# Optimization experiments

Measured on AMD Instinct MI355X. Metric: run time of the kernel, lower is better.

## Reference

```python
import jax, jax.numpy as jnp
import numpy as np

B, S, H, NH = 2, 2048, 1024, 16
DK = H // NH

def setup_inputs() -> dict:
    key = jax.random.key(0)
    ks = jax.random.split(key, 12)
    scale = 0.02
    return {
        "Q": jax.random.normal(ks[0], (B, S, H), jnp.float32),
        "K": jax.random.normal(ks[1], (B, S, H), jnp.float32),
        "V": jax.random.normal(ks[2], (B, S, H), jnp.float32),
        "attn_mask": jax.random.randint(ks[3], (B, S, S), 0, 2).astype(bool),
        "Wq": jax.random.normal(ks[4], (H, H), jnp.float32) * scale,
        "bq": jnp.zeros((H,), jnp.float32),
        "Wk": jax.random.normal(ks[5], (H, H), jnp.float32) * scale,
        "bk": jnp.zeros((H,), jnp.float32),
        "Wv": jax.random.normal(ks[6], (H, H), jnp.float32) * scale,
        "bv": jnp.zeros((H,), jnp.float32),
        "Wo": jax.random.normal(ks[7], (H, H), jnp.float32) * scale,
        "bo": jnp.zeros((H,), jnp.float32),
    }

def reference(Q, K, V, attn_mask, Wq, bq, Wk, bk, Wv, bv, Wo, bo):
    b = Q.shape[0]
    # linear projections (torch nn.Linear: x @ W.T + b), split heads -> [b, nh, s, dk]
    def proj(x, W, bias):
        return (x @ W.T + bias).reshape(b, -1, NH, DK).transpose(0, 2, 1, 3)
    q = proj(Q, Wq, bq)
    k = proj(K, Wk, bk)
    v = proj(V, Wv, bv)
    scores = jnp.einsum("bhqd,bhkd->bhqk", q, k) / jnp.sqrt(jnp.float32(DK))
    scores = jnp.where(attn_mask[:, None, :, :], jnp.float32(-1e9), scores)
    attn = jax.nn.softmax(scores, axis=-1)  # dropout prob = 0.0 (identity)
    ctx = jnp.einsum("bhqk,bhkd->bhqd", attn, v)
    ctx = ctx.transpose(0, 2, 1, 3).reshape(b, -1, NH * DK)
    return ctx @ Wo.T + bo
```

## Files before the change

### kernel.cpp

```cpp
#include <hip/hip_runtime.h>
#include <hip/hip_bf16.h>

typedef short s16x8 __attribute__((ext_vector_type(8)));
typedef float f32x4 __attribute__((ext_vector_type(4)));
typedef unsigned short u16;
typedef unsigned int u32;
typedef unsigned long long u64;

#define DEVI __device__ __forceinline__

#if __has_builtin(__builtin_amdgcn_exp2f)
#define EXP2F(x) __builtin_amdgcn_exp2f(x)
#else
#define EXP2F(x) exp2f(x)
#endif

#define QSCALE 0.1803368801111204f

DEVI float bf2f(u16 u){ union { u32 i; float f; } v; v.i = ((u32)u) << 16; return v.f; }
DEVI u16 f2bf(float f){ union { float f; u32 i; } v; v.f = f; u32 u = v.i;
                        return (u16)((u + 0x7fffu + ((u >> 16) & 1u)) >> 16); }

DEVI u32 pkbf2(float a, float b){
  union { __hip_bfloat162 h; u32 u; } v;
  v.h = __float22bfloat162_rn(make_float2(a, b));
  return v.u;
}
DEVI u64 pk4(float a, float b, float c, float d){
  return (u64)pkbf2(a, b) | ((u64)pkbf2(c, d) << 32);
}

DEVI f32x4 mfma_bf16(s16x8 a, s16x8 b, f32x4 c){
  return __builtin_amdgcn_mfma_f32_16x16x32_bf16(a, b, c, 0, 0, 0);
}

#define GLDS(gp, lp) __builtin_amdgcn_global_load_lds( \
    (const __attribute__((address_space(1))) void*)(gp), \
    (__attribute__((address_space(3))) void*)(lp), 16, 0, 0)

DEVI float4 cvt8f32(const float* p){
  float4 x = *(const float4*)p;
  float4 y = *(const float4*)(p + 4);
  union { u32 t[4]; float4 f4; } u;
  u.t[0] = pkbf2(x.x, x.y); u.t[1] = pkbf2(x.z, x.w);
  u.t[2] = pkbf2(y.x, y.y); u.t[3] = pkbf2(y.z, y.w);
  return u.f4;
}

DEVI bool detect_f32(const u16* probe){
  __shared__ int dsum[4];
  const int tid = threadIdx.x;
  int bad = 0;
#pragma unroll
  for (int i = 0; i < 16; ++i){
    u16 u = probe[tid * 16 + i];
    int e = (u >> 7) & 0xFF;
    bad += (e != 0 && (e < 100 || e > 150)) ? 1 : 0;
  }
#pragma unroll
  for (int o = 1; o < 64; o <<= 1) bad += __shfl_xor(bad, o);
  if ((tid & 63) == 0) dsum[tid >> 6] = bad;
  __syncthreads();
  bool r = (dsum[0] + dsum[1] + dsum[2] + dsum[3]) > 64;
  __syncthreads();
  return r;
}

struct PrepArgs { const void* src[7]; void* dst[7]; u32 coff[8]; };

__global__ __launch_bounds__(256) void prep_mask(PrepArgs a, const u16* probe,
                                                 const int* __restrict__ mask,
                                                 u64* __restrict__ bits,
                                                 int do_mask, int do_conv){
  if (blockIdx.x < 1024){
    if (!do_mask) return;
    const int lane = threadIdx.x & 63, wid = threadIdx.x >> 6;
    const int row = blockIdx.x * 4 + wid;
    const int* mrow = mask + (size_t)row * 2048;
    for (int c = 0; c < 32; ++c){
      int v = mrow[c * 64 + lane];
      u64 w = __ballot(v == 0);
      if (lane == 0) bits[(size_t)row * 32 + c] = w;
    }
  } else {
    if (!do_conv) return;
    const bool f32 = detect_f32(probe);
    if (!f32) return;
    const u32 total = a.coff[7];
    for (u32 c = (blockIdx.x - 1024) * 256 + threadIdx.x; c < total; c += 2048 * 256){
      int s = 0;
#pragma unroll
      for (int i = 1; i < 7; ++i) s += (c >= a.coff[i]) ? 1 : 0;
      u32 lc = c - a.coff[s];
      ((float4*)a.dst[s])[lc] = cvt8f32((const float*)a.src[s] + (size_t)lc * 8);
    }
  }
}

struct ProjP {
  const void* X[3];   const u16* Xc[3];
  const void* W[3];   const u16* Wc[3];
  const void* bias[3];
  u16* out[3];
  const u16* probe;
  int conv_ok;
};

__global__ __launch_bounds__(256) void proj_gemm(ProjP p){
  __shared__ u16 As[128 * 64];
  __shared__ u16 Bs[128 * 64];
  const int z = blockIdx.z;
  const bool in32 = detect_f32(p.probe);
  const bool f32st = in32 && !p.conv_ok;
  const u16* Ab = (in32 && p.conv_ok) ? p.Xc[z] : (const u16*)p.X[z];
  const u16* Wb = (in32 && p.conv_ok) ? p.Wc[z] : (const u16*)p.W[z];
  const float* Af = (const float*)p.X[z];
  const float* Wf = (const float*)p.W[z];
  const int tid = threadIdx.x;
  const int lane = tid & 63, wid = tid >> 6;
  const int quad = lane >> 4, l15 = lane & 15;
  const int m0 = blockIdx.y * 128, n0 = blockIdx.x * 128;
  const int wm = (wid >> 1) * 64, wn = (wid & 1) * 64;
  const int K = 1024;

  f32x4 acc[4][4];
  const f32x4 z4 = {0.f, 0.f, 0.f, 0.f};
  for (int i = 0; i < 4; ++i) for (int j = 0; j < 4; ++j) acc[i][j] = z4;

  for (int ko = 0; ko < 16; ++ko){
    const int kk = ko * 64;
    if (f32st){
#pragma unroll
      for (int i = 0; i < 4; ++i){
        int g = tid * 4 + i;
        int row = g >> 3, c = g & 7;
        *(float4*)(As + row * 64 + ((c ^ (row & 7)) * 8)) =
            cvt8f32(Af + (size_t)(m0 + row) * K + kk + c * 8);
        *(float4*)(Bs + row * 64 + ((c ^ (row & 7)) * 8)) =
            cvt8f32(Wf + (size_t)(n0 + row) * K + kk + c * 8);
      }
    } else {
#pragma unroll
      for (int i = 0; i < 4; ++i){
        int ci = (wid * 4 + i) * 64 + lane;
        int row = ci >> 3, gcc = (ci & 7) ^ (row & 7);
        GLDS(Ab + (size_t)(m0 + row) * K + kk + gcc * 8, As + (size_t)(wid * 4 + i) * 512);
        GLDS(Wb + (size_t)(n0 + row) * K + kk + gcc * 8, Bs + (size_t)(wid * 4 + i) * 512);
      }
    }
    __syncthreads();
#pragma unroll
    for (int ks = 0; ks < 2; ++ks){
      s16x8 af[4], bfr[4];
#pragma unroll
      for (int mt = 0; mt < 4; ++mt){
        int row = wm + mt * 16 + l15;
        af[mt] = *(const s16x8*)(As + row * 64 + (((ks * 4 + quad) ^ (row & 7)) * 8));
      }
#pragma unroll
      for (int nt = 0; nt < 4; ++nt){
        int row = wn + nt * 16 + l15;
        bfr[nt] = *(const s16x8*)(Bs + row * 64 + (((ks * 4 + quad) ^ (row & 7)) * 8));
      }
#pragma unroll
      for (int mt = 0; mt < 4; ++mt)
#pragma unroll
        for (int nt = 0; nt < 4; ++nt)
          acc[mt][nt] = mfma_bf16(af[mt], bfr[nt], acc[mt][nt]);
    }
    __syncthreads();
  }

  u16* outp = p.out[z];
#pragma unroll
  for (int nt = 0; nt < 4; ++nt){
    int col = n0 + wn + nt * 16 + l15;
    float bv = in32 ? ((const float*)p.bias[z])[col] : bf2f(((const u16*)p.bias[z])[col]);
#pragma unroll
    for (int mt = 0; mt < 4; ++mt){
      if (z == 2){
        int srow = m0 + wm + mt * 16 + quad * 4;
        int b = srow >> 11, s = srow & 2047, hh = col >> 6, d = col & 63;
        size_t idx = (((size_t)(b * 16 + hh)) * 64 + d) * 2048 + s;
        *(u64*)(outp + idx) = pk4(acc[mt][nt][0] + bv, acc[mt][nt][1] + bv,
                                  acc[mt][nt][2] + bv, acc[mt][nt][3] + bv);
      } else {
#pragma unroll
        for (int r = 0; r < 4; ++r){
          int row = m0 + wm + mt * 16 + quad * 4 + r;
          float v = acc[mt][nt][r] + bv;
          if (z == 0) v *= QSCALE;
          int b = row >> 11, s = row & 2047, hh = col >> 6, d = col & 63;
          outp[(((size_t)(b * 16 + hh)) * 2048 + s) * 64 + d] = f2bf(v);
        }
      }
    }
  }
}

__global__ __launch_bounds__(256) void gemm_out(const u16* __restrict__ A,
                                                const void* __restrict__ Wv,
                                                const u16* __restrict__ Wbf,
                                                const void* __restrict__ biasv,
                                                void* __restrict__ outv,
                                                const u16* __restrict__ probe,
                                                int conv_ok){
  __shared__ u16 As[64 * 64];
  __shared__ u16 Bs[64 * 64];
  const bool in32 = detect_f32(probe);
  const bool f32st = in32 && !conv_ok;
  const u16* Wb = (in32 && conv_ok) ? Wbf : (const u16*)Wv;
  const float* Wf = (const float*)Wv;
  const int tid = threadIdx.x;
  const int lane = tid & 63, wid = tid >> 6;
  const int quad = lane >> 4, l15 = lane & 15;
  const int m0 = blockIdx.y * 64, n0 = blockIdx.x * 64;
  const int wm = (wid >> 1) * 32, wn = (wid & 1) * 32;
  const int K = 1024;

  f32x4 acc[2][2];
  const f32x4 z4 = {0.f, 0.f, 0.f, 0.f};
  for (int i = 0; i < 2; ++i) for (int j = 0; j < 2; ++j) acc[i][j] = z4;

  for (int ko = 0; ko < 16; ++ko){
    const int kk = ko * 64;
#pragma unroll
    for (int i = 0; i < 2; ++i){
      int ci = (wid * 2 + i) * 64 + lane;
      int row = ci >> 3, gcc = (ci & 7) ^ (row & 7);
      GLDS(A + (size_t)(m0 + row) * K + kk + gcc * 8, As + (size_t)(wid * 2 + i) * 512);
    }
    if (f32st){
#pragma unroll
      for (int i = 0; i < 2; ++i){
        int g = tid * 2 + i;
        int row = g >> 3, c = g & 7;
        *(float4*)(Bs + row * 64 + ((c ^ (row & 7)) * 8)) =
            cvt8f32(Wf + (size_t)(n0 + row) * K + kk + c * 8);
      }
    } else {
#pragma unroll
      for (int i = 0; i < 2; ++i){
        int ci = (wid * 2 + i) * 64 + lane;
        int row = ci >> 3, gcc = (ci & 7) ^ (row & 7);
        GLDS(Wb + (size_t)(n0 + row) * K + kk + gcc * 8, Bs + (size_t)(wid * 2 + i) * 512);
      }
    }
    __syncthreads();
#pragma unroll
    for (int ks = 0; ks < 2; ++ks){
      s16x8 af[2], bfr[2];
#pragma unroll
      for (int mt = 0; mt < 2; ++mt){
        int row = wm + mt * 16 + l15;
        af[mt] = *(const s16x8*)(As + row * 64 + (((ks * 4 + quad) ^ (row & 7)) * 8));
      }
#pragma unroll
      for (int nt = 0; nt < 2; ++nt){
        int row = wn + nt * 16 + l15;
        bfr[nt] = *(const s16x8*)(Bs + row * 64 + (((ks * 4 + quad) ^ (row & 7)) * 8));
      }
#pragma unroll
      for (int mt = 0; mt < 2; ++mt)
#pragma unroll
        for (int nt = 0; nt < 2; ++nt)
          acc[mt][nt] = mfma_bf16(af[mt], bfr[nt], acc[mt][nt]);
    }
    __syncthreads();
  }

#pragma unroll
  for (int nt = 0; nt < 2; ++nt){
    int col = n0 + wn + nt * 16 + l15;
    float bv = in32 ? ((const float*)biasv)[col] : bf2f(((const u16*)biasv)[col]);
#pragma unroll
    for (int mt = 0; mt < 2; ++mt)
#pragma unroll
      for (int r = 0; r < 4; ++r){
        int row = m0 + wm + mt * 16 + quad * 4 + r;
        float v = acc[mt][nt][r] + bv;
        size_t idx = (size_t)row * 1024 + col;
        if (in32) ((float*)outv)[idx] = v;
        else      ((u16*)outv)[idx]   = f2bf(v);
      }
  }
}

__global__ __launch_bounds__(256, 2) void attn2(const u16* __restrict__ qws,
                                                const u16* __restrict__ kws,
                                                const u16* __restrict__ vtws,
                                                const u64* __restrict__ mbits,
                                                const int* __restrict__ rawmask,
                                                int use_raw,
                                                u16* __restrict__ ctxws){
  __shared__ u16 Ks[2][64 * 64];
  __shared__ u16 Vt[2][64 * 64];
  __shared__ u16 Ps[4][32 * 64];
  const int tid = threadIdx.x;
  const int lane = tid & 63, wid = tid >> 6;
  const int quad = lane >> 4, l15 = lane & 15;
  const int h = blockIdx.x, qt = blockIdx.y, b = blockIdx.z;
  const int q0 = qt * 128;
  const size_t bh = (size_t)(b * 16 + h) * (2048 * 64);
  int qrow[2];
  qrow[0] = q0 + wid * 32 + l15;
  qrow[1] = qrow[0] + 16;

  s16x8 qf[2][2];
#pragma unroll
  for (int rg = 0; rg < 2; ++rg)
#pragma unroll
    for (int ks = 0; ks < 2; ++ks)
      qf[rg][ks] = *(const s16x8*)(qws + bh + (size_t)qrow[rg] * 64 + ks * 32 + quad * 8);

  const f32x4 z4 = {0.f, 0.f, 0.f, 0.f};
  f32x4 ctx[2][4];
#pragma unroll
  for (int rg = 0; rg < 2; ++rg)
    for (int dt = 0; dt < 4; ++dt) ctx[rg][dt] = z4;
  float lr[2] = {0.f, 0.f};

  u16* pp = &Ps[wid][0];
  u32 pw[2][4];
#pragma unroll
  for (int rg = 0; rg < 2; ++rg)
#pragma unroll
    for (int ntk = 0; ntk < 4; ++ntk)
      pw[rg][ntk] = (rg * 16 + l15) * 64 +
                    (((u32)(ntk * 2 + (quad >> 1)) ^ (u32)(l15 & 7)) * 8) + (quad & 1) * 4;

  const u64* mrow0 = mbits + ((size_t)(b * 2048 + qrow[0])) * 32;
  const u64* mrow1 = mbits + ((size_t)(b * 2048 + qrow[1])) * 32;

  const int sci = wid * 2;
  int srow0, sgc0, srow1, sgc1;
  {
    int ci0 = sci * 64 + lane;
    srow0 = ci0 >> 3; sgc0 = (ci0 & 7) ^ (srow0 & 7);
    int ci1 = (sci + 1) * 64 + lane;
    srow1 = ci1 >> 3; sgc1 = (ci1 & 7) ^ (srow1 & 7);
  }
  const u16* kp0 = kws + bh + (size_t)srow0 * 64 + sgc0 * 8;
  const u16* kp1 = kws + bh + (size_t)srow1 * 64 + sgc1 * 8;
  const u16* vp0 = vtws + bh + (size_t)srow0 * 2048 + sgc0 * 8;
  const u16* vp1 = vtws + bh + (size_t)srow1 * 2048 + sgc1 * 8;

  GLDS(kp0, &Ks[0][0] + (size_t)sci * 512);
  GLDS(vp0, &Vt[0][0] + (size_t)sci * 512);
  GLDS(kp1, &Ks[0][0] + (size_t)(sci + 1) * 512);
  GLDS(vp1, &Vt[0][0] + (size_t)(sci + 1) * 512);
  kp0 += 4096; kp1 += 4096; vp0 += 64; vp1 += 64;

  for (int kt = 0; kt < 32; kt += 2){
#pragma unroll
    for (int hb = 0; hb < 2; ++hb){
      const int t = kt + hb;
      const u16* kb = &Ks[hb][0];
      const u16* vb = &Vt[hb][0];
      __syncthreads();

      u64 mw0 = 0, mw1 = 0;
      if (!use_raw){ mw0 = mrow0[t]; mw1 = mrow1[t]; }

      if (t < 31){
        u16* kd = &Ks[hb ^ 1][0];
        u16* vd = &Vt[hb ^ 1][0];
        GLDS(kp0, kd + (size_t)sci * 512);
        GLDS(vp0, vd + (size_t)sci * 512);
        GLDS(kp1, kd + (size_t)(sci + 1) * 512);
        GLDS(vp1, vd + (size_t)(sci + 1) * 512);
        kp0 += 4096; kp1 += 4096; vp0 += 64; vp1 += 64;
      }

      f32x4 s[2][4];
#pragma unroll
      for (int rg = 0; rg < 2; ++rg)
#pragma unroll
        for (int ntk = 0; ntk < 4; ++ntk) s[rg][ntk] = z4;
#pragma unroll
      for (int ks = 0; ks < 2; ++ks)
#pragma unroll
        for (int ntk = 0; ntk < 4; ++ntk){
          int row = ntk * 16 + l15;
          s16x8 kf = *(const s16x8*)(kb + row * 64 + (((ks * 4 + quad) ^ (row & 7)) * 8));
          s[0][ntk] = mfma_bf16(kf, qf[0][ks], s[0][ntk]);
          s[1][ntk] = mfma_bf16(kf, qf[1][ks], s[1][ntk]);
        }

      if (!use_raw){
#pragma unroll
        for (int rg = 0; rg < 2; ++rg){
          u64 w = (rg ? mw1 : mw0) >> (quad * 4);
          u32 wlo = (u32)w, whi = (u32)(w >> 32);
          float ls = 0.f;
#pragma unroll
          for (int ntk = 0; ntk < 4; ++ntk){
            u32 half32 = (ntk < 2) ? wlo : whi;
#pragma unroll
            for (int r = 0; r < 4; ++r){
              u32 keep = half32 & (1u << ((ntk & 1) * 16 + r));
              float sv = keep ? s[rg][ntk][r] : -1.0e9f;
              float pv = EXP2F(sv);
              s[rg][ntk][r] = pv;
              ls += pv;
            }
          }
          lr[rg] += ls;
        }
      } else {
        const int k0 = t * 64;
#pragma unroll
        for (int rg = 0; rg < 2; ++rg){
          float ls = 0.f;
#pragma unroll
          for (int ntk = 0; ntk < 4; ++ntk)
#pragma unroll
            for (int r = 0; r < 4; ++r){
              int key = k0 + ntk * 16 + quad * 4 + r;
              int mv = rawmask[((size_t)(b * 2048 + qrow[rg])) * 2048 + key];
              float pv = EXP2F(mv ? -1.0e9f : s[rg][ntk][r]);
              s[rg][ntk][r] = pv;
              ls += pv;
            }
          lr[rg] += ls;
        }
      }

#pragma unroll
      for (int rg = 0; rg < 2; ++rg)
#pragma unroll
        for (int ntk = 0; ntk < 4; ++ntk){
          uint2 tt;
          tt.x = pkbf2(s[rg][ntk][0], s[rg][ntk][1]);
          tt.y = pkbf2(s[rg][ntk][2], s[rg][ntk][3]);
          *(uint2*)(pp + pw[rg][ntk]) = tt;
        }
      s16x8 pf[2][2];
#pragma unroll
      for (int rg = 0; rg < 2; ++rg)
#pragma unroll
        for (int ks = 0; ks < 2; ++ks)
          pf[rg][ks] = *(const s16x8*)(pp + (rg * 16 + l15) * 64 +
                                       (((ks * 4 + quad) ^ (l15 & 7)) * 8));

#pragma unroll
      for (int ks = 0; ks < 2; ++ks)
#pragma unroll
        for (int dt = 0; dt < 4; ++dt){
          int row = dt * 16 + l15;
          s16x8 vf = *(const s16x8*)(vb + row * 64 + (((ks * 4 + quad) ^ (row & 7)) * 8));
          ctx[0][dt] = mfma_bf16(vf, pf[0][ks], ctx[0][dt]);
          ctx[1][dt] = mfma_bf16(vf, pf[1][ks], ctx[1][dt]);
        }
    }
  }

#pragma unroll
  for (int rg = 0; rg < 2; ++rg){
    lr[rg] += __shfl_xor(lr[rg], 16);
    lr[rg] += __shfl_xor(lr[rg], 32);
    float inv = 1.0f / fmaxf(lr[rg], 1e-30f);
#pragma unroll
    for (int dt = 0; dt < 4; ++dt){
      int d0 = dt * 16 + quad * 4;
      u64 w = pk4(ctx[rg][dt][0] * inv, ctx[rg][dt][1] * inv,
                  ctx[rg][dt][2] * inv, ctx[rg][dt][3] * inv);
      *(u64*)(ctxws + ((size_t)(b * 2048 + qrow[rg])) * 1024 + h * 64 + d0) = w;
    }
  }
}

extern "C" void kernel_launch(void* const* d_in, const int* in_sizes, int n_in,
                              void* d_out, int out_size, void* d_ws, size_t ws_size,
                              hipStream_t stream){
  const void* Q    = d_in[0];
  const void* Kin  = d_in[1];
  const void* Vin  = d_in[2];
  const int* mask  = (const int*)d_in[3];
  const void* Wq = d_in[4];  const void* bq = d_in[5];
  const void* Wk = d_in[6];  const void* bk = d_in[7];
  const void* Wv = d_in[8];  const void* bv = d_in[9];
  const void* Wo = d_in[10]; const void* bo = d_in[11];

  char* ws = (char*)d_ws;
  const size_t MB = 1u << 20;
  const bool small_ws = ws_size < 33 * MB;
  const bool big_ws   = ws_size >= 66 * MB;
  u64* mbits = (u64*)ws;
  const size_t base = small_ws ? 0 : MB;
  u16* qws  = (u16*)(ws + base);
  u16* kws  = (u16*)(ws + base + 8 * MB);
  u16* vtws = (u16*)(ws + base + 16 * MB);
  u16* cws  = (u16*)(ws + base + 24 * MB);
  u16* Qc  = (u16*)(ws + 33 * MB);
  u16* Kc  = (u16*)(ws + 41 * MB);
  u16* Vc  = (u16*)(ws + 49 * MB);
  u16* Wqc = (u16*)(ws + 57 * MB);
  u16* Wkc = (u16*)(ws + 59 * MB);
  u16* Wvc = (u16*)(ws + 61 * MB);
  u16* Woc = (u16*)(ws + 63 * MB);
  const u16* probe = (const u16*)Q;

  PrepArgs pa;
  pa.src[0] = Q;  pa.src[1] = Kin; pa.src[2] = Vin;
  pa.src[3] = Wq; pa.src[4] = Wk;  pa.src[5] = Wv; pa.src[6] = Wo;
  pa.dst[0] = Qc;  pa.dst[1] = Kc;  pa.dst[2] = Vc;
  pa.dst[3] = Wqc; pa.dst[4] = Wkc; pa.dst[5] = Wvc; pa.dst[6] = Woc;
  const u32 cq = 4194304 / 8, cw = 1048576 / 8;
  pa.coff[0] = 0;
  pa.coff[1] = cq;          pa.coff[2] = 2 * cq;      pa.coff[3] = 3 * cq;
  pa.coff[4] = 3 * cq + cw; pa.coff[5] = 3 * cq + 2 * cw;
  pa.coff[6] = 3 * cq + 3 * cw; pa.coff[7] = 3 * cq + 4 * cw;
  prep_mask<<<dim3(3072), 256, 0, stream>>>(pa, probe, mask, mbits,
                                            small_ws ? 0 : 1, big_ws ? 1 : 0);

  ProjP pp;
  pp.X[0] = Q;  pp.X[1] = Kin; pp.X[2] = Vin;
  pp.Xc[0] = Qc; pp.Xc[1] = Kc; pp.Xc[2] = Vc;
  pp.W[0] = Wq; pp.W[1] = Wk; pp.W[2] = Wv;
  pp.Wc[0] = Wqc; pp.Wc[1] = Wkc; pp.Wc[2] = Wvc;
  pp.bias[0] = bq; pp.bias[1] = bk; pp.bias[2] = bv;
  pp.out[0] = qws; pp.out[1] = kws; pp.out[2] = vtws;
  pp.probe = probe;
  pp.conv_ok = big_ws ? 1 : 0;
  proj_gemm<<<dim3(8, 32, 3), 256, 0, stream>>>(pp);

  attn2<<<dim3(16, 16, 2), 256, 0, stream>>>(qws, kws, vtws, mbits, mask,
                                             small_ws ? 1 : 0, cws);

  gemm_out<<<dim3(16, 64), 256, 0, stream>>>(cws, Wo, Woc, bo, d_out, probe,
                                             big_ws ? 1 : 0);
}
```

Measured before the change: 279.7 us.

## Load K/V fragments straight to registers, drop LDS staging and barriers

Result: slower. 346.2 us (+23.8%).

```diff
diff --git a/kernel.cpp b/kernel.cpp
--- a/kernel.cpp
+++ b/kernel.cpp
@@ -286,6 +286,111 @@
   }
 }
 
+#define ATT_TILE(T, KC, KN)                                                   \
+  do {                                                                        \
+    const int t_ = (T);                                                       \
+    u64 mw0 = 0, mw1 = 0;                                                     \
+    if (!use_raw){ mw0 = mrow0[t_]; mw1 = mrow1[t_]; }                        \
+       \
+    s16x8 vf[8];                                                              \
+    {                                                                         \
+      const u16* vtb = vbp + (size_t)t_ * 64;                                 \
+      _Pragma("unroll")                                                       \
+      for (int ks = 0; ks < 2; ++ks)                                          \
+        _Pragma("unroll")                                                     \
+        for (int dt = 0; dt < 4; ++dt)                                        \
+          vf[ks * 4 + dt] = *(const s16x8*)(vtb + vo[dt] + ks * 32);          \
+    }                                                                         \
+    f32x4 sv[2][4];                                                           \
+    _Pragma("unroll")                                                         \
+    for (int rg = 0; rg < 2; ++rg)                                            \
+      _Pragma("unroll")                                                       \
+      for (int n = 0; n < 4; ++n) sv[rg][n] = z4;                             \
+    __builtin_amdgcn_s_setprio(1);                                            \
+    _Pragma("unroll")                                                         \
+    for (int ks = 0; ks < 2; ++ks)                                            \
+      _Pragma("unroll")                                                       \
+      for (int n = 0; n < 4; ++n){                                            \
+        sv[0][n] = mfma_bf16(KC[ks * 4 + n], qf[0][ks], sv[0][n]);            \
+        sv[1][n] = mfma_bf16(KC[ks * 4 + n], qf[1][ks], sv[1][n]);            \
+      }                                                                       \
+    __builtin_amdgcn_s_setprio(0);                                            \
+        \
+    {                                                                         \
+      const u16* knb = kbp + (size_t)(t_ + 1) * 4096;                         \
+      _Pragma("unroll")                                                       \
+      for (int ks = 0; ks < 2; ++ks)                                          \
+        _Pragma("unroll")                                                     \
+        for (int n = 0; n < 4; ++n)                                           \
+          KN[ks * 4 + n] = *(const s16x8*)(knb + ko[n] + ks * 32);            \
+    }                                                                         \
+                \
+    if (!use_raw){                                                            \
+      _Pragma("unroll")                                                       \
+      for (int rg = 0; rg < 2; ++rg){                                         \
+        u64 w = (rg ? mw1 : mw0) >> (quad * 4);                               \
+        u32 wlo = (u32)w, whi = (u32)(w >> 32);                               \
+        float ls = 0.f;                                                       \
+        _Pragma("unroll")                                                     \
+        for (int n = 0; n < 4; ++n){                                          \
+          u32 half32 = (n < 2) ? wlo : whi;                                   \
+          _Pragma("unroll")                                                   \
+          for (int r = 0; r < 4; ++r){                                        \
+            u32 keep = half32 & (1u << ((n & 1) * 16 + r));                   \
+            float svv = keep ? sv[rg][n][r] : -1.0e9f;                        \
+            float pv = EXP2F(svv);                                            \
+            sv[rg][n][r] = pv;                                                \
+            ls += pv;                                                         \
+          }                                                                   \
+        }                                                                     \
+        lr[rg] += ls;                                                         \
+      }                                                                       \
+    } else {                                                                  \
+      const int k0 = t_ * 64;                                                 \
+      _Pragma("unroll")                                                       \
+      for (int rg = 0; rg < 2; ++rg){                                         \
+        float ls = 0.f;                                                       \
+        _Pragma("unroll")                                                     \
+        for (int n = 0; n < 4; ++n)                                           \
+          _Pragma("unroll")                                                   \
+          for (int r = 0; r < 4; ++r){                                        \
+            int key = k0 + n * 16 + quad * 4 + r;                             \
+            int mv = rawmask[((size_t)(b * 2048 + qrow[rg])) * 2048 + key];   \
+            float pv = EXP2F(mv ? -1.0e9f : sv[rg][n][r]);                    \
+            sv[rg][n][r] = pv;                                                \
+            ls += pv;                                                         \
+          }                                                                   \
+        lr[rg] += ls;                                                         \
+      }                                                                       \
+    }                                                                         \
+                        \
+    _Pragma("unroll")                                                         \
+    for (int rg = 0; rg < 2; ++rg)                                            \
+      _Pragma("unroll")                                                       \
+      for (int n = 0; n < 4; ++n){                                            \
+        uint2 tt;                                                             \
+        tt.x = pkbf2(sv[rg][n][0], sv[rg][n][1]);                             \
+        tt.y = pkbf2(sv[rg][n][2], sv[rg][n][3]);                             \
+        *(uint2*)(pp + pw[rg][n]) = tt;                                       \
+      }                                                                       \
+    s16x8 pf[2][2];                                                           \
+    _Pragma("unroll")                                                         \
+    for (int rg = 0; rg < 2; ++rg)                                            \
+      _Pragma("unroll")                                                       \
+      for (int ks = 0; ks < 2; ++ks)                                          \
+        pf[rg][ks] = *(const s16x8*)(pp + (rg * 16 + l15) * 64 +              \
+                                     (((ks * 4 + quad) ^ (l15 & 7)) * 8));    \
+    __builtin_amdgcn_s_setprio(1);                                            \
+    _Pragma("unroll")                                                         \
+    for (int ks = 0; ks < 2; ++ks)                                            \
+      _Pragma("unroll")                                                       \
+      for (int dt = 0; dt < 4; ++dt){                                         \
+        ctx[0][dt] = mfma_bf16(vf[ks * 4 + dt], pf[0][ks], ctx[0][dt]);       \
+        ctx[1][dt] = mfma_bf16(vf[ks * 4 + dt], pf[1][ks], ctx[1][dt]);       \
+      }                                                                       \
+    __builtin_amdgcn_s_setprio(0);                                            \
+  } while (0)
+
 __global__ __launch_bounds__(256, 2) void attn2(const u16* __restrict__ qws,
                                                 const u16* __restrict__ kws,
                                                 const u16* __restrict__ vtws,
@@ -293,13 +398,13 @@
                                                 const int* __restrict__ rawmask,
                                                 int use_raw,
                                                 u16* __restrict__ ctxws){
-  __shared__ u16 Ks[2][64 * 64];
-  __shared__ u16 Vt[2][64 * 64];
   __shared__ u16 Ps[4][32 * 64];
   const int tid = threadIdx.x;
   const int lane = tid & 63, wid = tid >> 6;
   const int quad = lane >> 4, l15 = lane & 15;
-  const int h = blockIdx.x, qt = blockIdx.y, b = blockIdx.z;
+  const int bid = blockIdx.x;
+  const int p = bid & 31, qt = bid >> 5;
+  const int h = p & 15, b = p >> 4;
   const int q0 = qt * 128;
   const size_t bh = (size_t)(b * 16 + h) * (2048 * 64);
   int qrow[2];
@@ -332,127 +437,25 @@
   const u64* mrow0 = mbits + ((size_t)(b * 2048 + qrow[0])) * 32;
   const u64* mrow1 = mbits + ((size_t)(b * 2048 + qrow[1])) * 32;
 
-  const int sci = wid * 2;
-  int srow0, sgc0, srow1, sgc1;
-  {
-    int ci0 = sci * 64 + lane;
-    srow0 = ci0 >> 3; sgc0 = (ci0 & 7) ^ (srow0 & 7);
-    int ci1 = (sci + 1) * 64 + lane;
-    srow1 = ci1 >> 3; sgc1 = (ci1 & 7) ^ (srow1 & 7);
-  }
-  const u16* kp0 = kws + bh + (size_t)srow0 * 64 + sgc0 * 8;
-  const u16* kp1 = kws + bh + (size_t)srow1 * 64 + sgc1 * 8;
-  const u16* vp0 = vtws + bh + (size_t)srow0 * 2048 + sgc0 * 8;
-  const u16* vp1 = vtws + bh + (size_t)srow1 * 2048 + sgc1 * 8;
-
-  GLDS(kp0, &Ks[0][0] + (size_t)sci * 512);
-  GLDS(vp0, &Vt[0][0] + (size_t)sci * 512);
-  GLDS(kp1, &Ks[0][0] + (size_t)(sci + 1) * 512);
-  GLDS(vp1, &Vt[0][0] + (size_t)(sci + 1) * 512);
-  kp0 += 4096; kp1 += 4096; vp0 += 64; vp1 += 64;
+  const u16* kbp = kws + bh;
+  const u16* vbp = vtws + bh;
+  u32 ko[4], vo[4];
+#pragma unroll
+  for (int i = 0; i < 4; ++i){
+    ko[i] = (u32)(i * 16 + l15) * 64 + quad * 8;
+    vo[i] = (u32)(i * 16 + l15) * 2048 + quad * 8;
+  }
+
+  s16x8 kfa[8], kfb[8];
+#pragma unroll
+  for (int ks = 0; ks < 2; ++ks)
+#pragma unroll
+    for (int n = 0; n < 4; ++n)
+      kfa[ks * 4 + n] = *(const s16x8*)(kbp + ko[n] + ks * 32);
 
   for (int kt = 0; kt < 32; kt += 2){
-#pragma unroll
-    for (int hb = 0; hb < 2; ++hb){
-      const int t = kt + hb;
-      const u16* kb = &Ks[hb][0];
-      const u16* vb = &Vt[hb][0];
-      __syncthreads();
-
-      u64 mw0 = 0, mw1 = 0;
-      if (!use_raw){ mw0 = mrow0[t]; mw1 = mrow1[t]; }
-
-      if (t < 31){
-        u16* kd = &Ks[hb ^ 1][0];
-        u16* vd = &Vt[hb ^ 1][0];
-        GLDS(kp0, kd + (size_t)sci * 512);
-        GLDS(vp0, vd + (size_t)sci * 512);
-        GLDS(kp1, kd + (size_t)(sci + 1) * 512);
-        GLDS(vp1, vd + (size_t)(sci + 1) * 512);
-        kp0 += 4096; kp1 += 4096; vp0 += 64; vp1 += 64;
-      }
-
-      f32x4 s[2][4];
-#pragma unroll
-      for (int rg = 0; rg < 2; ++rg)
-#pragma unroll
-        for (int ntk = 0; ntk < 4; ++ntk) s[rg][ntk] = z4;
-#pragma unroll
-      for (int ks = 0; ks < 2; ++ks)
-#pragma unroll
-        for (int ntk = 0; ntk < 4; ++ntk){
-          int row = ntk * 16 + l15;
-          s16x8 kf = *(const s16x8*)(kb + row * 64 + (((ks * 4 + quad) ^ (row & 7)) * 8));
-          s[0][ntk] = mfma_bf16(kf, qf[0][ks], s[0][ntk]);
-          s[1][ntk] = mfma_bf16(kf, qf[1][ks], s[1][ntk]);
-        }
-
-      if (!use_raw){
-#pragma unroll
-        for (int rg = 0; rg < 2; ++rg){
-          u64 w = (rg ? mw1 : mw0) >> (quad * 4);
-          u32 wlo = (u32)w, whi = (u32)(w >> 32);
-          float ls = 0.f;
-#pragma unroll
-          for (int ntk = 0; ntk < 4; ++ntk){
-            u32 half32 = (ntk < 2) ? wlo : whi;
-#pragma unroll
-            for (int r = 0; r < 4; ++r){
-              u32 keep = half32 & (1u << ((ntk & 1) * 16 + r));
-              float sv = keep ? s[rg][ntk][r] : -1.0e9f;
-              float pv = EXP2F(sv);
-              s[rg][ntk][r] = pv;
-              ls += pv;
-            }
-          }
-          lr[rg] += ls;
-        }
-      } else {
-        const int k0 = t * 64;
-#pragma unroll
-        for (int rg = 0; rg < 2; ++rg){
-          float ls = 0.f;
-#pragma unroll
-          for (int ntk = 0; ntk < 4; ++ntk)
-#pragma unroll
-            for (int r = 0; r < 4; ++r){
-              int key = k0 + ntk * 16 + quad * 4 + r;
-              int mv = rawmask[((size_t)(b * 2048 + qrow[rg])) * 2048 + key];
-              float pv = EXP2F(mv ? -1.0e9f : s[rg][ntk][r]);
-              s[rg][ntk][r] = pv;
-              ls += pv;
-            }
-          lr[rg] += ls;
-        }
-      }
-
-#pragma unroll
-      for (int rg = 0; rg < 2; ++rg)
-#pragma unroll
-        for (int ntk = 0; ntk < 4; ++ntk){
-          uint2 tt;
-          tt.x = pkbf2(s[rg][ntk][0], s[rg][ntk][1]);
-          tt.y = pkbf2(s[rg][ntk][2], s[rg][ntk][3]);
-          *(uint2*)(pp + pw[rg][ntk]) = tt;
-        }
-      s16x8 pf[2][2];
-#pragma unroll
-      for (int rg = 0; rg < 2; ++rg)
-#pragma unroll
-        for (int ks = 0; ks < 2; ++ks)
-          pf[rg][ks] = *(const s16x8*)(pp + (rg * 16 + l15) * 64 +
-                                       (((ks * 4 + quad) ^ (l15 & 7)) * 8));
-
-#pragma unroll
-      for (int ks = 0; ks < 2; ++ks)
-#pragma unroll
-        for (int dt = 0; dt < 4; ++dt){
-          int row = dt * 16 + l15;
-          s16x8 vf = *(const s16x8*)(vb + row * 64 + (((ks * 4 + quad) ^ (row & 7)) * 8));
-          ctx[0][dt] = mfma_bf16(vf, pf[0][ks], ctx[0][dt]);
-          ctx[1][dt] = mfma_bf16(vf, pf[1][ks], ctx[1][dt]);
-        }
-    }
+    ATT_TILE(kt, kfa, kfb);
+    ATT_TILE(kt + 1, kfb, kfa);
   }
 
 #pragma unroll
@@ -525,8 +528,8 @@
   pp.conv_ok = big_ws ? 1 : 0;
   proj_gemm<<<dim3(8, 32, 3), 256, 0, stream>>>(pp);
 
-  attn2<<<dim3(16, 16, 2), 256, 0, stream>>>(qws, kws, vtws, mbits, mask,
-                                             small_ws ? 1 : 0, cws);
+  attn2<<<dim3(512), 256, 0, stream>>>(qws, kws, vtws, mbits, mask,
+                                       small_ws ? 1 : 0, cws);
 
   gemm_out<<<dim3(16, 64), 256, 0, stream>>>(cws, Wo, Woc, bo, d_out, probe,
                                              big_ws ? 1 : 0);
```
